# Optimization experiments

Measured on AMD Instinct MI355X. Metric: run time of the kernel, lower is better.

## Reference

```python
import jax, jax.numpy as jnp
import numpy as np

FP8_E4M3_MAX = 448.0
EPS = 1.1920928955078125e-07  # torch.finfo(float32).eps, used by torchao amax_to_scale


def _fp8_quant(x):
    """Tensorwise dynamic fp8 (e4m3) quantization, torchao-style.
    Returns dequant-ready fp8 values (as fp32) and the scale."""
    amax = jnp.maximum(jnp.max(jnp.abs(x)), EPS)
    scale = FP8_E4M3_MAX / amax
    xq = jnp.clip(x * scale, -FP8_E4M3_MAX, FP8_E4M3_MAX)
    xq = xq.astype(jnp.float8_e4m3fn).astype(jnp.float32)
    return xq, scale


def setup_inputs() -> dict:
    key = jax.random.key(0)
    k1, k2 = jax.random.split(key)
    B, M, K, N = 8, 2048, 2048, 2048
    x = jax.random.normal(k1, (B, M, K), dtype=jnp.float32)
    weight = jax.random.normal(k2, (B, K, N), dtype=jnp.float32)  # kernel_initializer=normal_
    bias = jnp.zeros((B, 1, N), dtype=jnp.float32)  # bias_initializer=zeros_
    return {"x": x, "weight": weight, "bias": bias}


def reference(x, weight, bias):
    # per-tensor dynamic fp8 cast of input and weight
    xq, sx = _fp8_quant(x)
    wq, sw = _fp8_quant(weight)
    # batched fp8 GEMM with dequant: (xq/sx) @ (wq/sw)
    out = jnp.einsum("bmk,bkn->bmn", xq, wq) / (sx * sw)
    out = out + bias  # activation is None
    return out
```

## Files before the change

### kernel.cpp

```cpp
#include <hip/hip_runtime.h>
#include <cstdint>

#define FP8_MAX 448.0f
#define EPSF 1.1920928955078125e-07f

typedef float floatx4 __attribute__((ext_vector_type(4)));

#define BATCH 8
#define MDIM 2048
#define KDIM 2048
#define NDIM 2048
#define NELEM ((long)BATCH * MDIM * KDIM)
#define N4 (NELEM / 4)

#define QX_OFF 256
#define QW_OFF (256 + NELEM)

static __device__ __forceinline__ float wave_max(float v) {
    #pragma unroll
    for (int off = 32; off > 0; off >>= 1)
        v = fmaxf(v, __shfl_xor(v, off, 64));
    return v;
}

__global__ void amax_kernel(const float4* __restrict__ x, const float4* __restrict__ w,
                            unsigned int* __restrict__ amax) {
    const float4* p = blockIdx.y ? w : x;
    unsigned int* outp = amax + blockIdx.y;
    long idx = (long)blockIdx.x * blockDim.x + threadIdx.x;
    long stride = (long)gridDim.x * blockDim.x;
    float m = 0.f;
    for (long i = idx; i < N4; i += stride) {
        float4 v = p[i];
        m = fmaxf(m, fmaxf(fmaxf(fabsf(v.x), fabsf(v.y)), fmaxf(fabsf(v.z), fabsf(v.w))));
    }
    m = wave_max(m);
    __shared__ float smax[4];
    int lane = threadIdx.x & 63, wv = threadIdx.x >> 6;
    if (lane == 0) smax[wv] = m;
    __syncthreads();
    if (threadIdx.x == 0) {
        m = fmaxf(fmaxf(smax[0], smax[1]), fmaxf(smax[2], smax[3]));
        atomicMax(outp, __float_as_uint(m));
    }
}

static __device__ __forceinline__ uint32_t quant4(float4 v, float s) {
    float a = fminf(fmaxf(v.x * s, -FP8_MAX), FP8_MAX);
    float b = fminf(fmaxf(v.y * s, -FP8_MAX), FP8_MAX);
    float c = fminf(fmaxf(v.z * s, -FP8_MAX), FP8_MAX);
    float d = fminf(fmaxf(v.w * s, -FP8_MAX), FP8_MAX);
    uint32_t r = (uint32_t)__builtin_amdgcn_cvt_pk_fp8_f32(a, b, 0, false);
    r = (uint32_t)__builtin_amdgcn_cvt_pk_fp8_f32(c, d, (int)r, true);
    return r;
}

__global__ void quant_x_kernel(const float4* __restrict__ x, uint32_t* __restrict__ qx,
                               const unsigned int* __restrict__ amax) {
    float ax = fmaxf(__uint_as_float(amax[0]), EPSF);
    float s = FP8_MAX / ax;
    long idx = (long)blockIdx.x * blockDim.x + threadIdx.x;
    long stride = (long)gridDim.x * blockDim.x;
    for (long i = idx; i < N4; i += stride)
        qx[i] = quant4(x[i], s);
}

__global__ void quant_w_kernel(const float* __restrict__ w, uint8_t* __restrict__ qwT,
                               const unsigned int* __restrict__ amax) {
    float aw = fmaxf(__uint_as_float(amax[1]), EPSF);
    float s = FP8_MAX / aw;
    __shared__ uint8_t ldsT[64 * 68];
    int t = threadIdx.x;
    int n0 = blockIdx.x * 64, k0 = blockIdx.y * 64;
    long base = (long)blockIdx.z * KDIM * NDIM;
    int nl = (t & 15) * 4;
    int kl = t >> 4;
    #pragma unroll
    for (int it = 0; it < 4; ++it) {
        int k = kl + it * 16;
        float4 v = *(const float4*)(w + base + (long)(k0 + k) * NDIM + n0 + nl);
        uint32_t r = quant4(v, s);
        ldsT[(nl + 0) * 68 + k] = (uint8_t)(r);
        ldsT[(nl + 1) * 68 + k] = (uint8_t)(r >> 8);
        ldsT[(nl + 2) * 68 + k] = (uint8_t)(r >> 16);
        ldsT[(nl + 3) * 68 + k] = (uint8_t)(r >> 24);
    }
    __syncthreads();
    int n = t >> 2, c = t & 3;
    const uint8_t* src = &ldsT[n * 68 + c * 16];
    uint4 d;
    d.x = *(const uint32_t*)(src + 0);
    d.y = *(const uint32_t*)(src + 4);
    d.z = *(const uint32_t*)(src + 8);
    d.w = *(const uint32_t*)(src + 12);
    *(uint4*)(qwT + base + (long)(n0 + n) * KDIM + k0 + c * 16) = d;
}

#define BM 128
#define BN 128
#define BK 64

__global__ __launch_bounds__(256) void gemm_kernel(const uint8_t* __restrict__ qx,
                                                   const uint8_t* __restrict__ qwT,
                                                   const float* __restrict__ bias,
                                                   float* __restrict__ out,
                                                   const unsigned int* __restrict__ amax) {
    int b = blockIdx.z;
    int tm = blockIdx.y, tn = blockIdx.x;
    __shared__ uint8_t lA[BM * BK];
    __shared__ uint8_t lB[BN * BK];
    int t = threadIdx.x, lane = t & 63, wv = t >> 6;
    int wm = wv & 1, wn = wv >> 1;
    int m = lane & 15, g = lane >> 4;
    int ghi = g >> 1, glo8 = (g & 1) * 8;

    const uint8_t* Ab = qx + (long)b * MDIM * KDIM + (long)tm * BM * KDIM;
    const uint8_t* Bb = qwT + (long)b * NDIM * KDIM + (long)tn * BN * KDIM;

    floatx4 acc[4][4] = {};

    int lin0 = t, lin1 = 256 + t;
    int row0 = lin0 >> 2, row1 = lin1 >> 2;
    int src0 = ((lin0 & 3) ^ ((row0 >> 1) & 3)) * 16;
    int src1 = ((lin1 & 3) ^ ((row1 >> 1) & 3)) * 16;

    for (int kt = 0; kt < KDIM / BK; ++kt) {
        long k0 = (long)kt * BK;
        __builtin_amdgcn_global_load_lds(
            (const __attribute__((address_space(1))) uint32_t*)(Ab + (long)row0 * KDIM + k0 + src0),
            (__attribute__((address_space(3))) uint32_t*)(lA + lin0 * 16), 16, 0, 0);
        __builtin_amdgcn_global_load_lds(
            (const __attribute__((address_space(1))) uint32_t*)(Ab + (long)row1 * KDIM + k0 + src1),
            (__attribute__((address_space(3))) uint32_t*)(lA + lin1 * 16), 16, 0, 0);
        __builtin_amdgcn_global_load_lds(
            (const __attribute__((address_space(1))) uint32_t*)(Bb + (long)row0 * KDIM + k0 + src0),
            (__attribute__((address_space(3))) uint32_t*)(lB + lin0 * 16), 16, 0, 0);
        __builtin_amdgcn_global_load_lds(
            (const __attribute__((address_space(1))) uint32_t*)(Bb + (long)row1 * KDIM + k0 + src1),
            (__attribute__((address_space(3))) uint32_t*)(lB + lin1 * 16), 16, 0, 0);
        __syncthreads();

        #pragma unroll
        for (int kk = 0; kk < 2; ++kk) {
            int gc = kk * 2 + ghi;
            long a_frag[4], b_frag[4];
            #pragma unroll
            for (int mt = 0; mt < 4; ++mt) {
                int r = wm * 64 + mt * 16 + m;
                int pc = gc ^ ((r >> 1) & 3);
                a_frag[mt] = *(const long*)&lA[r * BK + pc * 16 + glo8];
            }
            #pragma unroll
            for (int nt = 0; nt < 4; ++nt) {
                int r = wn * 64 + nt * 16 + m;
                int pc = gc ^ ((r >> 1) & 3);
                b_frag[nt] = *(const long*)&lB[r * BK + pc * 16 + glo8];
            }
            #pragma unroll
            for (int mt = 0; mt < 4; ++mt)
                #pragma unroll
                for (int nt = 0; nt < 4; ++nt)
                    acc[mt][nt] = __builtin_amdgcn_mfma_f32_16x16x32_fp8_fp8(
                        a_frag[mt], b_frag[nt], acc[mt][nt], 0, 0, 0);
        }
        __syncthreads();
    }

    float ax = fmaxf(__uint_as_float(amax[0]), EPSF);
    float aw = fmaxf(__uint_as_float(amax[1]), EPSF);
    float ds = (ax / FP8_MAX) * (aw / FP8_MAX);

    #pragma unroll
    for (int mt = 0; mt < 4; ++mt) {
        #pragma unroll
        for (int nt = 0; nt < 4; ++nt) {
            int col = tn * BN + wn * 64 + nt * 16 + m;
            float bv = bias[(long)b * NDIM + col];
            int row0e = tm * BM + wm * 64 + mt * 16 + g * 4;
            #pragma unroll
            for (int r = 0; r < 4; ++r) {
                out[((long)b * MDIM + row0e + r) * NDIM + col] = acc[mt][nt][r] * ds + bv;
            }
        }
    }
}

extern "C" void kernel_launch(void* const* d_in, const int* in_sizes, int n_in,
                              void* d_out, int out_size, void* d_ws, size_t ws_size,
                              hipStream_t stream) {
    const float* x = (const float*)d_in[0];
    const float* w = (const float*)d_in[1];
    const float* bias = (const float*)d_in[2];
    float* out = (float*)d_out;

    unsigned int* amax = (unsigned int*)d_ws;
    uint8_t* qx = (uint8_t*)d_ws + QX_OFF;
    uint8_t* qwT = (uint8_t*)d_ws + QW_OFF;
    (void)in_sizes; (void)n_in; (void)out_size; (void)ws_size;

    hipMemsetAsync(d_ws, 0, 8, stream);

    amax_kernel<<<dim3(2048, 2), 256, 0, stream>>>((const float4*)x, (const float4*)w, amax);
    quant_x_kernel<<<8192, 256, 0, stream>>>((const float4*)x, (uint32_t*)qx, amax);
    quant_w_kernel<<<dim3(NDIM / 64, KDIM / 64, BATCH), 256, 0, stream>>>(w, qwT, amax);
    gemm_kernel<<<dim3(NDIM / BN, MDIM / BM, BATCH), 256, 0, stream>>>(qx, qwT, bias, out, amax);
}
```

Baseline: 504.5 us.

## Rewrite fp8 GEMM with 256x256 tiles, 8 waves and double-buffered LDS pipeline

The GEMM kernel moves from 128x128 tiles with 4 waves to 256x256 tiles with 8 waves. It double-buffers the K tiles in a 64 KB LDS region, issuing asynchronous global-to-LDS loads for the next stages while MFMAs run on the current one. Explicit waitcnt, barrier, sched_barrier and setprio calls interleave the loads with the compute phases. The aim is to hide memory latency and raise arithmetic intensity per block, at the cost of more registers and LDS per block, fewer blocks in the grid, and fragile hand-written synchronisation.

Result: faster. 487.9 us (-3.3%).

```diff
diff --git a/kernel.cpp b/kernel.cpp
--- a/kernel.cpp
+++ b/kernel.cpp
@@ -96,91 +96,149 @@
     *(uint4*)(qwT + base + (long)(n0 + n) * KDIM + k0 + c * 16) = d;
 }
 
-#define BM 128
-#define BN 128
+#define BM 256
+#define BN 256
 #define BK 64
-
-__global__ __launch_bounds__(256) void gemm_kernel(const uint8_t* __restrict__ qx,
-                                                   const uint8_t* __restrict__ qwT,
-                                                   const float* __restrict__ bias,
-                                                   float* __restrict__ out,
-                                                   const unsigned int* __restrict__ amax) {
+#define NT (KDIM / BK)
+
+__global__ __launch_bounds__(512, 2) void gemm_kernel(const uint8_t* __restrict__ qx,
+                                                      const uint8_t* __restrict__ qwT,
+                                                      const float* __restrict__ bias,
+                                                      float* __restrict__ out,
+                                                      const unsigned int* __restrict__ amax) {
     int b = blockIdx.z;
     int tm = blockIdx.y, tn = blockIdx.x;
-    __shared__ uint8_t lA[BM * BK];
-    __shared__ uint8_t lB[BN * BK];
+    __shared__ uint8_t lds[65536];
     int t = threadIdx.x, lane = t & 63, wv = t >> 6;
     int wm = wv & 1, wn = wv >> 1;
     int m = lane & 15, g = lane >> 4;
-    int ghi = g >> 1, glo8 = (g & 1) * 8;
+    int gh = g >> 1, glo8 = (g & 1) * 8;
 
     const uint8_t* Ab = qx + (long)b * MDIM * KDIM + (long)tm * BM * KDIM;
     const uint8_t* Bb = qwT + (long)b * NDIM * KDIM + (long)tn * BN * KDIM;
 
-    floatx4 acc[4][4] = {};
-
-    int lin0 = t, lin1 = 256 + t;
-    int row0 = lin0 >> 2, row1 = lin1 >> 2;
-    int src0 = ((lin0 & 3) ^ ((row0 >> 1) & 3)) * 16;
-    int src1 = ((lin1 & 3) ^ ((row1 >> 1) & 3)) * 16;
-
-    for (int kt = 0; kt < KDIM / BK; ++kt) {
-        long k0 = (long)kt * BK;
-        __builtin_amdgcn_global_load_lds(
-            (const __attribute__((address_space(1))) uint32_t*)(Ab + (long)row0 * KDIM + k0 + src0),
-            (__attribute__((address_space(3))) uint32_t*)(lA + lin0 * 16), 16, 0, 0);
-        __builtin_amdgcn_global_load_lds(
-            (const __attribute__((address_space(1))) uint32_t*)(Ab + (long)row1 * KDIM + k0 + src1),
-            (__attribute__((address_space(3))) uint32_t*)(lA + lin1 * 16), 16, 0, 0);
-        __builtin_amdgcn_global_load_lds(
-            (const __attribute__((address_space(1))) uint32_t*)(Bb + (long)row0 * KDIM + k0 + src0),
-            (__attribute__((address_space(3))) uint32_t*)(lB + lin0 * 16), 16, 0, 0);
-        __builtin_amdgcn_global_load_lds(
-            (const __attribute__((address_space(1))) uint32_t*)(Bb + (long)row1 * KDIM + k0 + src1),
-            (__attribute__((address_space(3))) uint32_t*)(lB + lin1 * 16), 16, 0, 0);
-        __syncthreads();
-
-        #pragma unroll
-        for (int kk = 0; kk < 2; ++kk) {
-            int gc = kk * 2 + ghi;
-            long a_frag[4], b_frag[4];
-            #pragma unroll
-            for (int mt = 0; mt < 4; ++mt) {
-                int r = wm * 64 + mt * 16 + m;
-                int pc = gc ^ ((r >> 1) & 3);
-                a_frag[mt] = *(const long*)&lA[r * BK + pc * 16 + glo8];
-            }
-            #pragma unroll
-            for (int nt = 0; nt < 4; ++nt) {
-                int r = wn * 64 + nt * 16 + m;
-                int pc = gc ^ ((r >> 1) & 3);
-                b_frag[nt] = *(const long*)&lB[r * BK + pc * 16 + glo8];
-            }
-            #pragma unroll
-            for (int mt = 0; mt < 4; ++mt)
-                #pragma unroll
-                for (int nt = 0; nt < 4; ++nt)
-                    acc[mt][nt] = __builtin_amdgcn_mfma_f32_16x16x32_fp8_fp8(
-                        a_frag[mt], b_frag[nt], acc[mt][nt], 0, 0, 0);
-        }
-        __syncthreads();
-    }
+    int srow = t >> 1;
+    int sc16 = ((t & 1) ^ ((srow >> 2) & 1)) * 16;
+    const uint8_t* asrc = Ab + (long)srow * KDIM + sc16;
+    const uint8_t* bsrc = Bb + (long)srow * KDIM + sc16;
+
+#define STAGE(s_, isB_, h_) do {                                                              \
+    const uint8_t* _src = ((isB_) ? bsrc : asrc) + (long)(s_) * BK + (h_) * 32;               \
+    __builtin_amdgcn_global_load_lds(                                                         \
+        (const __attribute__((address_space(1))) uint32_t*)_src,                              \
+        (__attribute__((address_space(3))) uint32_t*)(lds + (((s_) & 1) << 15) +              \
+            (isB_) * 16384 + (h_) * 8192 + t * 16), 16, 0, 0);                                \
+} while (0)
+
+    int aoff[8];
+    #pragma unroll
+    for (int mi = 0; mi < 8; ++mi) {
+        int r = wm * 128 + mi * 16 + m;
+        aoff[mi] = r * 32 + ((gh ^ ((r >> 2) & 1)) * 16) + glo8;
+    }
+    int boff[4];
+    #pragma unroll
+    for (int ni = 0; ni < 4; ++ni) {
+        int r = wn * 64 + ni * 16 + m;
+        boff[ni] = 16384 + r * 32 + ((gh ^ ((r >> 2) & 1)) * 16) + glo8;
+    }
+
+    floatx4 acc[8][4] = {};
+    long a0[8], bq[2];
+
+    STAGE(0, 0, 0); STAGE(0, 1, 0); STAGE(0, 0, 1); STAGE(0, 1, 1);
+    STAGE(1, 0, 0); STAGE(1, 1, 0);
+    asm volatile("s_waitcnt vmcnt(4)" ::: "memory");
+    __builtin_amdgcn_s_barrier();
+
+    #pragma unroll 2
+    for (int s = 0; s < NT; ++s) {
+        const uint8_t* L = lds + ((s & 1) << 15);
+
+        #pragma unroll
+        for (int mi = 0; mi < 8; ++mi) a0[mi] = *(const long*)(L + aoff[mi]);
+        bq[0] = *(const long*)(L + boff[0]);
+        bq[1] = *(const long*)(L + boff[1]);
+        if (s + 1 < NT) STAGE(s + 1, 0, 1);
+        __builtin_amdgcn_s_barrier();
+        asm volatile("s_waitcnt lgkmcnt(0)" ::: "memory");
+        __builtin_amdgcn_sched_barrier(0);
+        __builtin_amdgcn_s_setprio(1);
+        #pragma unroll
+        for (int mi = 0; mi < 8; ++mi) {
+            acc[mi][0] = __builtin_amdgcn_mfma_f32_16x16x32_fp8_fp8(a0[mi], bq[0], acc[mi][0], 0, 0, 0);
+            acc[mi][1] = __builtin_amdgcn_mfma_f32_16x16x32_fp8_fp8(a0[mi], bq[1], acc[mi][1], 0, 0, 0);
+        }
+        __builtin_amdgcn_s_setprio(0);
+        __builtin_amdgcn_s_barrier();
+
+        bq[0] = *(const long*)(L + boff[2]);
+        bq[1] = *(const long*)(L + boff[3]);
+        if (s + 1 < NT) STAGE(s + 1, 1, 1);
+        __builtin_amdgcn_s_barrier();
+        asm volatile("s_waitcnt lgkmcnt(0)" ::: "memory");
+        __builtin_amdgcn_sched_barrier(0);
+        __builtin_amdgcn_s_setprio(1);
+        #pragma unroll
+        for (int mi = 0; mi < 8; ++mi) {
+            acc[mi][2] = __builtin_amdgcn_mfma_f32_16x16x32_fp8_fp8(a0[mi], bq[0], acc[mi][2], 0, 0, 0);
+            acc[mi][3] = __builtin_amdgcn_mfma_f32_16x16x32_fp8_fp8(a0[mi], bq[1], acc[mi][3], 0, 0, 0);
+        }
+        __builtin_amdgcn_s_setprio(0);
+        if (s < NT - 1) asm volatile("s_waitcnt vmcnt(4)" ::: "memory");
+        else            asm volatile("s_waitcnt vmcnt(0)" ::: "memory");
+        __builtin_amdgcn_s_barrier();
+
+        #pragma unroll
+        for (int mi = 0; mi < 8; ++mi) a0[mi] = *(const long*)(L + 8192 + aoff[mi]);
+        bq[0] = *(const long*)(L + 8192 + boff[2]);
+        bq[1] = *(const long*)(L + 8192 + boff[3]);
+        if (s + 2 < NT) STAGE(s + 2, 0, 0);
+        __builtin_amdgcn_s_barrier();
+        asm volatile("s_waitcnt lgkmcnt(0)" ::: "memory");
+        __builtin_amdgcn_sched_barrier(0);
+        __builtin_amdgcn_s_setprio(1);
+        #pragma unroll
+        for (int mi = 0; mi < 8; ++mi) {
+            acc[mi][2] = __builtin_amdgcn_mfma_f32_16x16x32_fp8_fp8(a0[mi], bq[0], acc[mi][2], 0, 0, 0);
+            acc[mi][3] = __builtin_amdgcn_mfma_f32_16x16x32_fp8_fp8(a0[mi], bq[1], acc[mi][3], 0, 0, 0);
+        }
+        __builtin_amdgcn_s_setprio(0);
+        __builtin_amdgcn_s_barrier();
+
+        bq[0] = *(const long*)(L + 8192 + boff[0]);
+        bq[1] = *(const long*)(L + 8192 + boff[1]);
+        if (s + 2 < NT) STAGE(s + 2, 1, 0);
+        __builtin_amdgcn_s_barrier();
+        asm volatile("s_waitcnt lgkmcnt(0)" ::: "memory");
+        __builtin_amdgcn_sched_barrier(0);
+        __builtin_amdgcn_s_setprio(1);
+        #pragma unroll
+        for (int mi = 0; mi < 8; ++mi) {
+            acc[mi][0] = __builtin_amdgcn_mfma_f32_16x16x32_fp8_fp8(a0[mi], bq[0], acc[mi][0], 0, 0, 0);
+            acc[mi][1] = __builtin_amdgcn_mfma_f32_16x16x32_fp8_fp8(a0[mi], bq[1], acc[mi][1], 0, 0, 0);
+        }
+        __builtin_amdgcn_s_setprio(0);
+        if (s < NT - 2)       asm volatile("s_waitcnt vmcnt(4)" ::: "memory");
+        else if (s == NT - 2) asm volatile("s_waitcnt vmcnt(2)" ::: "memory");
+        __builtin_amdgcn_s_barrier();
+    }
+#undef STAGE
 
     float ax = fmaxf(__uint_as_float(amax[0]), EPSF);
     float aw = fmaxf(__uint_as_float(amax[1]), EPSF);
-    float ds = (ax / FP8_MAX) * (aw / FP8_MAX);
-
-    #pragma unroll
-    for (int mt = 0; mt < 4; ++mt) {
-        #pragma unroll
-        for (int nt = 0; nt < 4; ++nt) {
-            int col = tn * BN + wn * 64 + nt * 16 + m;
-            float bv = bias[(long)b * NDIM + col];
-            int row0e = tm * BM + wm * 64 + mt * 16 + g * 4;
+    float dsc = (ax / FP8_MAX) * (aw / FP8_MAX);
+
+    #pragma unroll
+    for (int ni = 0; ni < 4; ++ni) {
+        int col = tn * BN + wn * 64 + ni * 16 + m;
+        float bv = bias[(long)b * NDIM + col];
+        #pragma unroll
+        for (int mi = 0; mi < 8; ++mi) {
+            int row0 = tm * BM + wm * 128 + mi * 16 + g * 4;
             #pragma unroll
-            for (int r = 0; r < 4; ++r) {
-                out[((long)b * MDIM + row0e + r) * NDIM + col] = acc[mt][nt][r] * ds + bv;
-            }
+            for (int r = 0; r < 4; ++r)
+                out[((long)b * MDIM + row0 + r) * NDIM + col] = acc[mi][ni][r] * dsc + bv;
         }
     }
 }
@@ -203,5 +261,5 @@
     amax_kernel<<<dim3(2048, 2), 256, 0, stream>>>((const float4*)x, (const float4*)w, amax);
     quant_x_kernel<<<8192, 256, 0, stream>>>((const float4*)x, (uint32_t*)qx, amax);
     quant_w_kernel<<<dim3(NDIM / 64, KDIM / 64, BATCH), 256, 0, stream>>>(w, qwT, amax);
-    gemm_kernel<<<dim3(NDIM / BN, MDIM / BM, BATCH), 256, 0, stream>>>(qx, qwT, bias, out, amax);
-}
+    gemm_kernel<<<dim3(NDIM / BN, MDIM / BM, BATCH), 512, 0, stream>>>(qx, qwT, bias, out, amax);
+}
```

## Rewrite fp8 GEMM with 256x256 tiles, 32x32x64 MFMA, triple-buffered LDS pipeline

Applied to the files above, without the earlier changes.

The GEMM moves to 256x256 block tiles with 512 threads, the gfx950 scaled 32x32x64 f8f6f4 MFMA (unit scales), and a three-stage LDS ring of asynchronous global-to-LDS loads that prefetches two k-tiles ahead, with explicit waitcnt and barrier control plus raised wave priority around the MFMA block. The aim is to raise arithmetic intensity per byte loaded and to hide global load latency behind compute. The amax and quant_x kernels now run fixed, unrolled iteration counts in place of grid-stride loops. The cost is higher register and LDS use (96KB shared) and correctness that depends on hardcoded sizes and hand-placed waitcnt values.

After: 454.9 us. 9.8% less time.

```diff
diff --git a/kernel.cpp b/kernel.cpp
--- a/kernel.cpp
+++ b/kernel.cpp
@@ -5,6 +5,9 @@
 #define EPSF 1.1920928955078125e-07f
 
 typedef float floatx4 __attribute__((ext_vector_type(4)));
+typedef float floatx16 __attribute__((ext_vector_type(16)));
+typedef int intx4 __attribute__((ext_vector_type(4)));
+typedef int intx8 __attribute__((ext_vector_type(8)));
 
 #define BATCH 8
 #define MDIM 2048
@@ -23,18 +26,22 @@
     return v;
 }
 
+#define AMAX_BLOCKS 2048
 __global__ void amax_kernel(const float4* __restrict__ x, const float4* __restrict__ w,
                             unsigned int* __restrict__ amax) {
     const float4* p = blockIdx.y ? w : x;
     unsigned int* outp = amax + blockIdx.y;
     long idx = (long)blockIdx.x * blockDim.x + threadIdx.x;
-    long stride = (long)gridDim.x * blockDim.x;
-    float m = 0.f;
-    for (long i = idx; i < N4; i += stride) {
-        float4 v = p[i];
-        m = fmaxf(m, fmaxf(fmaxf(fabsf(v.x), fabsf(v.y)), fmaxf(fabsf(v.z), fabsf(v.w))));
-    }
-    m = wave_max(m);
+    const long stride = (long)AMAX_BLOCKS * 256;
+    float m0 = 0.f, m1 = 0.f;
+    #pragma unroll
+    for (int it = 0; it < 16; it += 2) {
+        float4 v0 = p[idx + (long)it * stride];
+        float4 v1 = p[idx + (long)(it + 1) * stride];
+        m0 = fmaxf(m0, fmaxf(fmaxf(fabsf(v0.x), fabsf(v0.y)), fmaxf(fabsf(v0.z), fabsf(v0.w))));
+        m1 = fmaxf(m1, fmaxf(fmaxf(fabsf(v1.x), fabsf(v1.y)), fmaxf(fabsf(v1.z), fabsf(v1.w))));
+    }
+    float m = wave_max(fmaxf(m0, m1));
     __shared__ float smax[4];
     int lane = threadIdx.x & 63, wv = threadIdx.x >> 6;
     if (lane == 0) smax[wv] = m;
@@ -55,14 +62,18 @@
     return r;
 }
 
+#define QX_BLOCKS 8192
 __global__ void quant_x_kernel(const float4* __restrict__ x, uint32_t* __restrict__ qx,
                                const unsigned int* __restrict__ amax) {
     float ax = fmaxf(__uint_as_float(amax[0]), EPSF);
     float s = FP8_MAX / ax;
     long idx = (long)blockIdx.x * blockDim.x + threadIdx.x;
-    long stride = (long)gridDim.x * blockDim.x;
-    for (long i = idx; i < N4; i += stride)
+    const long stride = (long)QX_BLOCKS * 256;
+    #pragma unroll
+    for (int it = 0; it < 4; ++it) {
+        long i = idx + (long)it * stride;
         qx[i] = quant4(x[i], s);
+    }
 }
 
 __global__ void quant_w_kernel(const float* __restrict__ w, uint8_t* __restrict__ qwT,
@@ -96,90 +107,118 @@
     *(uint4*)(qwT + base + (long)(n0 + n) * KDIM + k0 + c * 16) = d;
 }
 
-#define BM 128
-#define BN 128
+#define BM 256
+#define BN 256
 #define BK 64
-
-__global__ __launch_bounds__(256) void gemm_kernel(const uint8_t* __restrict__ qx,
-                                                   const uint8_t* __restrict__ qwT,
-                                                   const float* __restrict__ bias,
-                                                   float* __restrict__ out,
-                                                   const unsigned int* __restrict__ amax) {
+#define NT (KDIM / BK)
+
+__global__ __launch_bounds__(512, 2) void gemm_kernel(const uint8_t* __restrict__ qx,
+                                                      const uint8_t* __restrict__ qwT,
+                                                      const float* __restrict__ bias,
+                                                      float* __restrict__ out,
+                                                      const unsigned int* __restrict__ amax) {
     int b = blockIdx.z;
     int tm = blockIdx.y, tn = blockIdx.x;
-    __shared__ uint8_t lA[BM * BK];
-    __shared__ uint8_t lB[BN * BK];
+    __shared__ uint8_t lds[98304];
     int t = threadIdx.x, lane = t & 63, wv = t >> 6;
-    int wm = wv & 1, wn = wv >> 1;
-    int m = lane & 15, g = lane >> 4;
-    int ghi = g >> 1, glo8 = (g & 1) * 8;
+    int wm = wv >> 2, wn = wv & 3;
+    int rl = lane & 31, kh = lane >> 5;
 
     const uint8_t* Ab = qx + (long)b * MDIM * KDIM + (long)tm * BM * KDIM;
     const uint8_t* Bb = qwT + (long)b * NDIM * KDIM + (long)tn * BN * KDIM;
 
-    floatx4 acc[4][4] = {};
-
-    int lin0 = t, lin1 = 256 + t;
-    int row0 = lin0 >> 2, row1 = lin1 >> 2;
-    int src0 = ((lin0 & 3) ^ ((row0 >> 1) & 3)) * 16;
-    int src1 = ((lin1 & 3) ^ ((row1 >> 1) & 3)) * 16;
-
-    for (int kt = 0; kt < KDIM / BK; ++kt) {
-        long k0 = (long)kt * BK;
-        __builtin_amdgcn_global_load_lds(
-            (const __attribute__((address_space(1))) uint32_t*)(Ab + (long)row0 * KDIM + k0 + src0),
-            (__attribute__((address_space(3))) uint32_t*)(lA + lin0 * 16), 16, 0, 0);
-        __builtin_amdgcn_global_load_lds(
-            (const __attribute__((address_space(1))) uint32_t*)(Ab + (long)row1 * KDIM + k0 + src1),
-            (__attribute__((address_space(3))) uint32_t*)(lA + lin1 * 16), 16, 0, 0);
-        __builtin_amdgcn_global_load_lds(
-            (const __attribute__((address_space(1))) uint32_t*)(Bb + (long)row0 * KDIM + k0 + src0),
-            (__attribute__((address_space(3))) uint32_t*)(lB + lin0 * 16), 16, 0, 0);
-        __builtin_amdgcn_global_load_lds(
-            (const __attribute__((address_space(1))) uint32_t*)(Bb + (long)row1 * KDIM + k0 + src1),
-            (__attribute__((address_space(3))) uint32_t*)(lB + lin1 * 16), 16, 0, 0);
-        __syncthreads();
-
-        #pragma unroll
-        for (int kk = 0; kk < 2; ++kk) {
-            int gc = kk * 2 + ghi;
-            long a_frag[4], b_frag[4];
+    long stoff = (long)(t >> 2) * KDIM + (long)(((t & 3) ^ ((t >> 3) & 3)) << 4);
+
+#define STAGE(base_, isB_, u_, kt_) do {                                                      \
+    const uint8_t* _s = ((isB_) ? Bb : Ab) + stoff + (long)(u_) * (128L * KDIM)               \
+                        + (long)(kt_) * BK;                                                   \
+    __builtin_amdgcn_global_load_lds(                                                         \
+        (const __attribute__((address_space(1))) uint32_t*)_s,                                \
+        (__attribute__((address_space(3))) uint32_t*)(lds + (base_) + (isB_) * 16384 +        \
+            (u_) * 8192 + t * 16), 16, 0, 0);                                                 \
+} while (0)
+
+    int aoff[4];
+    #pragma unroll
+    for (int mi = 0; mi < 4; ++mi) {
+        int r = wm * 128 + mi * 32 + rl;
+        aoff[mi] = r * 64 + ((((kh * 2) ^ ((r >> 1) & 3))) << 4);
+    }
+    int boff[2];
+    #pragma unroll
+    for (int ni = 0; ni < 2; ++ni) {
+        int r = wn * 64 + ni * 32 + rl;
+        boff[ni] = 16384 + r * 64 + ((((kh * 2) ^ ((r >> 1) & 3))) << 4);
+    }
+
+    floatx16 acc[4][2] = {};
+
+    STAGE(0, 0, 0, 0); STAGE(0, 0, 1, 0); STAGE(0, 1, 0, 0); STAGE(0, 1, 1, 0);
+    STAGE(32768, 0, 0, 1); STAGE(32768, 0, 1, 1); STAGE(32768, 1, 0, 1); STAGE(32768, 1, 1, 1);
+    asm volatile("s_waitcnt vmcnt(4)" ::: "memory");
+    __builtin_amdgcn_s_barrier();
+
+    int buf = 0;
+    for (int s = 0; s < NT; ++s) {
+        const uint8_t* L = lds + buf * 32768;
+
+        intx8 af[4], bf[2];
+        #pragma unroll
+        for (int mi = 0; mi < 4; ++mi) {
+            intx4 lo = *(const intx4*)(L + aoff[mi]);
+            intx4 hi = *(const intx4*)(L + (aoff[mi] ^ 16));
+            af[mi] = __builtin_shufflevector(lo, hi, 0, 1, 2, 3, 4, 5, 6, 7);
+        }
+        #pragma unroll
+        for (int ni = 0; ni < 2; ++ni) {
+            intx4 lo = *(const intx4*)(L + boff[ni]);
+            intx4 hi = *(const intx4*)(L + (boff[ni] ^ 16));
+            bf[ni] = __builtin_shufflevector(lo, hi, 0, 1, 2, 3, 4, 5, 6, 7);
+        }
+
+        int buf2 = (buf >= 1) ? buf - 1 : 2;
+        if (s + 2 < NT) {
+            STAGE(buf2 * 32768, 0, 0, s + 2); STAGE(buf2 * 32768, 0, 1, s + 2);
+            STAGE(buf2 * 32768, 1, 0, s + 2); STAGE(buf2 * 32768, 1, 1, s + 2);
+        }
+
+        __builtin_amdgcn_s_barrier();
+        asm volatile("s_waitcnt lgkmcnt(0)" ::: "memory");
+        __builtin_amdgcn_sched_barrier(0);
+        __builtin_amdgcn_s_setprio(1);
+        #pragma unroll
+        for (int mi = 0; mi < 4; ++mi) {
             #pragma unroll
-            for (int mt = 0; mt < 4; ++mt) {
-                int r = wm * 64 + mt * 16 + m;
-                int pc = gc ^ ((r >> 1) & 3);
-                a_frag[mt] = *(const long*)&lA[r * BK + pc * 16 + glo8];
+            for (int ni = 0; ni < 2; ++ni) {
+                acc[mi][ni] = __builtin_amdgcn_mfma_scale_f32_32x32x64_f8f6f4(
+                    af[mi], bf[ni], acc[mi][ni], 0, 0,
+                    0, 0x7f7f7f7f, 0, 0x7f7f7f7f);
             }
-            #pragma unroll
-            for (int nt = 0; nt < 4; ++nt) {
-                int r = wn * 64 + nt * 16 + m;
-                int pc = gc ^ ((r >> 1) & 3);
-                b_frag[nt] = *(const long*)&lB[r * BK + pc * 16 + glo8];
-            }
-            #pragma unroll
-            for (int mt = 0; mt < 4; ++mt)
-                #pragma unroll
-                for (int nt = 0; nt < 4; ++nt)
-                    acc[mt][nt] = __builtin_amdgcn_mfma_f32_16x16x32_fp8_fp8(
-                        a_frag[mt], b_frag[nt], acc[mt][nt], 0, 0, 0);
-        }
-        __syncthreads();
-    }
+        }
+        __builtin_amdgcn_s_setprio(0);
+
+        if (s < NT - 2)       asm volatile("s_waitcnt vmcnt(4)" ::: "memory");
+        else if (s == NT - 2) asm volatile("s_waitcnt vmcnt(0)" ::: "memory");
+        __builtin_amdgcn_s_barrier();
+        buf = (buf == 2) ? 0 : buf + 1;
+    }
+#undef STAGE
 
     float ax = fmaxf(__uint_as_float(amax[0]), EPSF);
     float aw = fmaxf(__uint_as_float(amax[1]), EPSF);
-    float ds = (ax / FP8_MAX) * (aw / FP8_MAX);
-
-    #pragma unroll
-    for (int mt = 0; mt < 4; ++mt) {
-        #pragma unroll
-        for (int nt = 0; nt < 4; ++nt) {
-            int col = tn * BN + wn * 64 + nt * 16 + m;
-            float bv = bias[(long)b * NDIM + col];
-            int row0e = tm * BM + wm * 64 + mt * 16 + g * 4;
+    float dsc = (ax / FP8_MAX) * (aw / FP8_MAX);
+
+    #pragma unroll
+    for (int ni = 0; ni < 2; ++ni) {
+        int col = tn * BN + wn * 64 + ni * 32 + rl;
+        float bv = bias[(long)b * NDIM + col];
+        #pragma unroll
+        for (int mi = 0; mi < 4; ++mi) {
+            int rbase = tm * BM + wm * 128 + mi * 32 + kh * 4;
             #pragma unroll
-            for (int r = 0; r < 4; ++r) {
-                out[((long)b * MDIM + row0e + r) * NDIM + col] = acc[mt][nt][r] * ds + bv;
+            for (int r = 0; r < 16; ++r) {
+                int grow = rbase + (r & 3) + 8 * (r >> 2);
+                out[((long)b * MDIM + grow) * NDIM + col] = acc[mi][ni][r] * dsc + bv;
             }
         }
     }
@@ -200,8 +239,8 @@
 
     hipMemsetAsync(d_ws, 0, 8, stream);
 
-    amax_kernel<<<dim3(2048, 2), 256, 0, stream>>>((const float4*)x, (const float4*)w, amax);
-    quant_x_kernel<<<8192, 256, 0, stream>>>((const float4*)x, (uint32_t*)qx, amax);
+    amax_kernel<<<dim3(AMAX_BLOCKS, 2), 256, 0, stream>>>((const float4*)x, (const float4*)w, amax);
+    quant_x_kernel<<<QX_BLOCKS, 256, 0, stream>>>((const float4*)x, (uint32_t*)qx, amax);
     quant_w_kernel<<<dim3(NDIM / 64, KDIM / 64, BATCH), 256, 0, stream>>>(w, qwT, amax);
-    gemm_kernel<<<dim3(NDIM / BN, MDIM / BM, BATCH), 256, 0, stream>>>(qx, qwT, bias, out, amax);
-}
+    gemm_kernel<<<dim3(NDIM / BN, MDIM / BM, BATCH), 512, 0, stream>>>(qx, qwT, bias, out, amax);
+}
```
